# Kernel optimization log

Hardware: AMD Instinct MI355X
Metric: run time of the kernel (lower is better)

Reference implementation:

```python
import jax, jax.numpy as jnp
import numpy as np

D_MODEL = 1024
N_HEADS = 16
D_HEAD = D_MODEL // N_HEADS
SCALE = D_HEAD ** -0.5


def setup_inputs() -> dict:
    key = jax.random.key(0)
    ks = jax.random.split(key, 9)
    s = 0.02
    x = jax.random.normal(ks[0], (2, 2048, D_MODEL), dtype=jnp.float32)
    Wq = jax.random.normal(ks[1], (D_MODEL, D_MODEL), dtype=jnp.float32) * s
    Wk = jax.random.normal(ks[2], (D_MODEL, D_MODEL), dtype=jnp.float32) * s
    Wv = jax.random.normal(ks[3], (D_MODEL, D_MODEL), dtype=jnp.float32) * s
    Wo = jax.random.normal(ks[4], (D_MODEL, D_MODEL), dtype=jnp.float32) * s
    bq = jax.random.normal(ks[5], (D_MODEL,), dtype=jnp.float32) * s
    bk = jax.random.normal(ks[6], (D_MODEL,), dtype=jnp.float32) * s
    bv = jax.random.normal(ks[7], (D_MODEL,), dtype=jnp.float32) * s
    bo = jax.random.normal(ks[8], (D_MODEL,), dtype=jnp.float32) * s
    return {"x": x, "Wq": Wq, "bq": bq, "Wk": Wk, "bk": bk,
            "Wv": Wv, "bv": bv, "Wo": Wo, "bo": bo}


def reference(x, Wq, bq, Wk, bk, Wv, bv, Wo, bo):
    B, S, _ = x.shape
    # torch nn.Linear: y = x @ W.T + b
    def proj(W, b):
        h = jnp.einsum('bsd,ed->bse', x, W) + b
        return h.reshape(B, S, N_HEADS, D_HEAD).transpose(0, 2, 1, 3)  # [B,H,S,Dh]
    Q = proj(Wq, bq)
    K = proj(Wk, bk)
    V = proj(Wv, bv)
    # chunked QK^T softmax over full K == full attention (no mask, dropout=0)
    scores = jnp.einsum('bhqd,bhkd->bhqk', Q, K) * SCALE  # [B,H,S,S]
    attn = jax.nn.softmax(scores, axis=-1)
    out = jnp.einsum('bhqk,bhkd->bhqd', attn, V)
    out = out.transpose(0, 2, 1, 3).reshape(B, S, D_MODEL)
    return jnp.einsum('bsd,ed->bse', out, Wo) + bo
```

## Files before the change

### kernel.cpp

```cpp
#include <hip/hip_runtime.h>
#include <cstdint>
#include <cstddef>


typedef unsigned short u16;
typedef unsigned int u32;
typedef __bf16 bf16x8 __attribute__((ext_vector_type(8)));
typedef float f32x4 __attribute__((ext_vector_type(4)));

#define GLOAD_LDS16(gp, lp)                                                            \
  __builtin_amdgcn_global_load_lds((const __attribute__((address_space(1))) void*)(gp),\
                                   (__attribute__((address_space(3))) void*)(lp),      \
                                   16, 0, 0)

__device__ __forceinline__ u16 f2bf(float f) {
  unsigned u = __builtin_bit_cast(unsigned, f);
  u = u + 0x7fffu + ((u >> 16) & 1u);
  return (u16)(u >> 16);
}

__device__ __forceinline__ u32 pack_bf2(float a, float b) {
  u32 ua = __builtin_bit_cast(u32, a) + 0x8000u;
  u32 ub = __builtin_bit_cast(u32, b) + 0x8000u;
  return __builtin_amdgcn_perm(ub, ua, 0x07060302u);
}

#define QSCALE 0.1803368801111204f

__global__ void cvt_all(const float* __restrict__ x,
                        const float* __restrict__ wq, const float* __restrict__ wk,
                        const float* __restrict__ wv, const float* __restrict__ wo,
                        u16* __restrict__ xb, u16* __restrict__ wqb,
                        u16* __restrict__ wkb, u16* __restrict__ wvb,
                        u16* __restrict__ wob) {
  int bx = blockIdx.x;
  const float* s; u16* d; int off;
  if (bx < 2048)      { s = x;  d = xb;  off = bx; }
  else if (bx < 2560) { s = wq; d = wqb; off = bx - 2048; }
  else if (bx < 3072) { s = wk; d = wkb; off = bx - 2560; }
  else if (bx < 3584) { s = wv; d = wvb; off = bx - 3072; }
  else                { s = wo; d = wob; off = bx - 3584; }
  int i = off * 2048 + threadIdx.x * 8;
  float4 a = *(const float4*)(s + i);
  float4 b = *(const float4*)(s + i + 4);
  uint4 o;
  o.x = f2bf(a.x) | ((u32)f2bf(a.y) << 16);
  o.y = f2bf(a.z) | ((u32)f2bf(a.w) << 16);
  o.z = f2bf(b.x) | ((u32)f2bf(b.y) << 16);
  o.w = f2bf(b.z) | ((u32)f2bf(b.w) << 16);
  *(uint4*)(d + i) = o;
}

template <int MODE>
__global__ __launch_bounds__(256, 3) void gemm_mfma(
    const u16* __restrict__ A,
    const u16* __restrict__ W0, const u16* __restrict__ W1, const u16* __restrict__ W2,
    const float* __restrict__ b0, const float* __restrict__ b1, const float* __restrict__ b2,
    u16* __restrict__ o0, u16* __restrict__ o1, u16* __restrict__ o2,
    float* __restrict__ oF)
{
  __shared__ __align__(16) u16 As[128 * 64];
  __shared__ __align__(16) u16 Bs[128 * 64];

  const int tid = threadIdx.x;
  const int w = tid >> 6, l = tid & 63;
  const int lane = l & 15, quad = l >> 4;
  const int wm = w >> 1, wn = w & 1;
  const int m0 = blockIdx.y * 128;
  const int n0g = blockIdx.x * 128;

  const int src = (MODE == 0) ? (n0g >> 10) : 0;
  const u16* Wsel = (MODE == 0) ? (src == 0 ? W0 : (src == 1 ? W1 : W2)) : W0;
  const float* bsel = (MODE == 0) ? (src == 0 ? b0 : (src == 1 ? b1 : b2)) : b0;
  const int n_base = (MODE == 0) ? (n0g & 1023) : n0g;

  const int c8 = ((l & 7) ^ (l >> 3)) * 8;

  f32x4 acc[4][4] = {};

  for (int kt = 0; kt < 1024; kt += 64) {
    __syncthreads();
    const u16* Ag = A + (size_t)m0 * 1024 + kt;
    const u16* Bg = Wsel + (size_t)n_base * 1024 + kt;
    #pragma unroll
    for (int i = 0; i < 4; ++i) {
      int rr = w * 32 + i * 8;
      GLOAD_LDS16(Ag + (size_t)(rr + (l >> 3)) * 1024 + c8, As + rr * 64);
      GLOAD_LDS16(Bg + (size_t)(rr + (l >> 3)) * 1024 + c8, Bs + rr * 64);
    }
    __syncthreads();

    bf16x8 af[4][2], bf[4][2];
    #pragma unroll
    for (int mf = 0; mf < 4; ++mf)
      #pragma unroll
      for (int ks = 0; ks < 2; ++ks) {
        af[mf][ks] = *(const bf16x8*)((const char*)As +
            (wm * 64 + mf * 16 + lane) * 128 + (((ks * 4 + quad) ^ (lane & 7)) * 16));
        bf[mf][ks] = *(const bf16x8*)((const char*)Bs +
            (wn * 64 + mf * 16 + lane) * 128 + (((ks * 4 + quad) ^ (lane & 7)) * 16));
      }
    #pragma unroll
    for (int ks = 0; ks < 2; ++ks)
      #pragma unroll
      for (int mf = 0; mf < 4; ++mf)
        #pragma unroll
        for (int nf = 0; nf < 4; ++nf)
          acc[mf][nf] = __builtin_amdgcn_mfma_f32_16x16x32_bf16(
              af[mf][ks], bf[nf][ks], acc[mf][nf], 0, 0, 0);
  }

  float bb[4];
  #pragma unroll
  for (int nf = 0; nf < 4; ++nf) bb[nf] = bsel[n_base + wn * 64 + nf * 16 + lane];

  u16* osel = (MODE == 0) ? (src == 0 ? o0 : (src == 1 ? o1 : o2)) : o0;

  #pragma unroll
  for (int mf = 0; mf < 4; ++mf) {
    int mb = m0 + wm * 64 + mf * 16 + quad * 4;
    #pragma unroll
    for (int nf = 0; nf < 4; ++nf) {
      int n_l = wn * 64 + nf * 16 + lane;
      if (MODE == 0 && src == 2) {
        float v0 = acc[mf][nf][0] + bb[nf];
        float v1 = acc[mf][nf][1] + bb[nf];
        float v2 = acc[mf][nf][2] + bb[nf];
        float v3 = acc[mf][nf][3] + bb[nf];
        int bi = mb >> 11, s = mb & 2047;
        int n_in = n_base + n_l;
        int h = n_in >> 6, dh = n_in & 63;
        uint2 pk = make_uint2(pack_bf2(v0, v1), pack_bf2(v2, v3));
        *(uint2*)(o2 + (((size_t)(bi * 16 + h) * 64 + dh) * 2048 + s)) = pk;
      } else {
        #pragma unroll
        for (int r = 0; r < 4; ++r) {
          float v = acc[mf][nf][r] + bb[nf];
          int m = mb + r;
          if (MODE == 0) {
            if (src == 0) v *= QSCALE;
            int bi = m >> 11, s = m & 2047;
            int n_in = n_base + n_l;
            int h = n_in >> 6, dh = n_in & 63;
            osel[(((size_t)(bi * 16 + h) * 2048 + s) << 6) + dh] = f2bf(v);
          } else {
            oF[(size_t)m * 1024 + n0g + n_l] = v;
          }
        }
      }
    }
  }
}

union SMemU {
  struct {
    u16 K[2][64 * 64];
    u16 V[2][64 * 64];
    u16 P[4][32 * 64];
  } m;
  struct {
    float O[4][32 * 64];
    float L[4][32];
  } f;
};

__global__ __launch_bounds__(512, 4) void attn_mfma(
    const u16* __restrict__ Qg_, const u16* __restrict__ Kg_,
    const u16* __restrict__ VTg_, u16* __restrict__ Og)
{
  __shared__ __align__(16) SMemU sm;

  const int tid = threadIdx.x;
  const int w = tid >> 6, l = tid & 63;
  const int lane = l & 15, quad = l >> 4;
  const int g = w >> 1;
  const int kh = w & 1;
  const int bh = blockIdx.y;
  const int q0 = blockIdx.x * 128;

  const u16* Qg  = Qg_ + ((size_t)bh * 2048 + q0 + g * 32) * 64;
  const u16* Kg  = Kg_ + (size_t)bh * 2048 * 64;
  const u16* VTg = VTg_ + (size_t)bh * 64 * 2048;

  const int c8 = ((l & 7) ^ (l >> 3)) * 8;
  const int lrow = l >> 3;
  const int rr = w * 8;

  bf16x8 bq[2][2];
  #pragma unroll
  for (int qf = 0; qf < 2; ++qf)
    #pragma unroll
    for (int ks = 0; ks < 2; ++ks)
      bq[qf][ks] = *(const bf16x8*)(Qg +
          (size_t)(qf * 16 + lane) * 64 + ks * 32 + quad * 8);

  GLOAD_LDS16(Kg + (size_t)(rr + lrow) * 64 + c8, sm.m.K[0] + rr * 64);
  GLOAD_LDS16(VTg + (size_t)(rr + lrow) * 2048 + c8, sm.m.V[0] + rr * 64);

  f32x4 oa[2][4] = {};
  float lsum[2] = {0.f, 0.f};
  u16* Pp = sm.m.P[g];

  for (int kt = 0; kt < 32; ++kt) {
    const int buf = kt & 1;
    __syncthreads();

    if (kt < 31) {
      GLOAD_LDS16(Kg + (size_t)((kt + 1) * 64 + rr + lrow) * 64 + c8,
                  sm.m.K[buf ^ 1] + rr * 64);
      GLOAD_LDS16(VTg + (size_t)(rr + lrow) * 2048 + (kt + 1) * 64 + c8,
                  sm.m.V[buf ^ 1] + rr * 64);
    }

    f32x4 sa[2][2] = {};
    #pragma unroll
    for (int ks = 0; ks < 2; ++ks) {
      bf16x8 ak[2];
      #pragma unroll
      for (int kf = 0; kf < 2; ++kf)
        ak[kf] = *(const bf16x8*)((const char*)sm.m.K[buf] +
            (kh * 32 + kf * 16 + lane) * 128 + (((ks * 4 + quad) ^ (lane & 7)) * 16));
      #pragma unroll
      for (int kf = 0; kf < 2; ++kf)
        #pragma unroll
        for (int qf = 0; qf < 2; ++qf)
          sa[kf][qf] = __builtin_amdgcn_mfma_f32_16x16x32_bf16(
              ak[kf], bq[qf][ks], sa[kf][qf], 0, 0, 0);
    }

    #pragma unroll
    for (int qf = 0; qf < 2; ++qf) {
      int qrow = qf * 16 + lane;
      #pragma unroll
      for (int kf = 0; kf < 2; ++kf) {
        float p0 = __builtin_amdgcn_exp2f(sa[kf][qf][0]);
        float p1 = __builtin_amdgcn_exp2f(sa[kf][qf][1]);
        float p2 = __builtin_amdgcn_exp2f(sa[kf][qf][2]);
        float p3 = __builtin_amdgcn_exp2f(sa[kf][qf][3]);
        lsum[qf] += (p0 + p1) + (p2 + p3);
        int c = kh * 4 + kf * 2 + (quad >> 1);
        *(uint2*)((char*)Pp + qrow * 128 + ((c ^ (lane & 7)) * 16) + (quad & 1) * 8)
            = make_uint2(pack_bf2(p0, p1), pack_bf2(p2, p3));
      }
    }

    {
      bf16x8 bv[4];
      #pragma unroll
      for (int df = 0; df < 4; ++df)
        bv[df] = *(const bf16x8*)((const char*)sm.m.V[buf] +
            (df * 16 + lane) * 128 + (((kh * 4 + quad) ^ (lane & 7)) * 16));
      bf16x8 ap[2];
      #pragma unroll
      for (int qf = 0; qf < 2; ++qf)
        ap[qf] = *(const bf16x8*)((const char*)Pp +
            (qf * 16 + lane) * 128 + (((kh * 4 + quad) ^ (lane & 7)) * 16));
      #pragma unroll
      for (int qf = 0; qf < 2; ++qf)
        #pragma unroll
        for (int df = 0; df < 4; ++df)
          oa[qf][df] = __builtin_amdgcn_mfma_f32_16x16x32_bf16(
              ap[qf], bv[df], oa[qf][df], 0, 0, 0);
    }
  }

  #pragma unroll
  for (int qf = 0; qf < 2; ++qf) {
    lsum[qf] += __shfl_xor(lsum[qf], 16);
    lsum[qf] += __shfl_xor(lsum[qf], 32);
  }

  __syncthreads();
  if (kh == 1) {
    #pragma unroll
    for (int qf = 0; qf < 2; ++qf)
      #pragma unroll
      for (int df = 0; df < 4; ++df)
        #pragma unroll
        for (int r = 0; r < 4; ++r)
          sm.f.O[g][(qf * 16 + quad * 4 + r) * 64 + df * 16 + lane] = oa[qf][df][r];
    if (l < 16) {
      sm.f.L[g][l] = lsum[0];
      sm.f.L[g][16 + l] = lsum[1];
    }
  }
  __syncthreads();
  if (kh == 0) {
    const int b = bh >> 4, hh = bh & 15;
    u16* Ob = Og + ((size_t)b * 2048 + q0 + g * 32) * 1024 + hh * 64;
    float ltot[2];
    #pragma unroll
    for (int qf = 0; qf < 2; ++qf)
      ltot[qf] = lsum[qf] + sm.f.L[g][qf * 16 + lane];
    #pragma unroll
    for (int qf = 0; qf < 2; ++qf)
      #pragma unroll
      for (int r = 0; r < 4; ++r) {
        float inv = 1.0f / __shfl(ltot[qf], quad * 4 + r, 16);
        int qrow = qf * 16 + quad * 4 + r;
        #pragma unroll
        for (int df = 0; df < 4; ++df) {
          float v = oa[qf][df][r] + sm.f.O[g][qrow * 64 + df * 16 + lane];
          Ob[(size_t)qrow * 1024 + df * 16 + lane] = f2bf(v * inv);
        }
      }
  }
}

extern "C" void kernel_launch(void* const* d_in, const int* in_sizes, int n_in,
                              void* d_out, int out_size, void* d_ws, size_t ws_size,
                              hipStream_t stream)
{
  (void)in_sizes; (void)n_in; (void)out_size; (void)ws_size;
  const float* x  = (const float*)d_in[0];
  const float* Wq = (const float*)d_in[1];
  const float* bq = (const float*)d_in[2];
  const float* Wk = (const float*)d_in[3];
  const float* bk = (const float*)d_in[4];
  const float* Wv = (const float*)d_in[5];
  const float* bv = (const float*)d_in[6];
  const float* Wo = (const float*)d_in[7];
  const float* bo = (const float*)d_in[8];
  float* y = (float*)d_out;

  const size_t NM = (size_t)4096 * 1024;
  u16* xb  = (u16*)d_ws;
  u16* wqb = xb + NM;
  u16* wkb = wqb + 1024 * 1024;
  u16* wvb = wkb + 1024 * 1024;
  u16* wob = wvb + 1024 * 1024;
  u16* Qb  = wob + 1024 * 1024;
  u16* Kb  = Qb + NM;
  u16* VTb = Kb + NM;
  u16* AOb = VTb + NM;

  cvt_all<<<4096, 256, 0, stream>>>(x, Wq, Wk, Wv, Wo, xb, wqb, wkb, wvb, wob);

  gemm_mfma<0><<<dim3(24, 32), 256, 0, stream>>>(
      xb, wqb, wkb, wvb, bq, bk, bv, Qb, Kb, VTb, nullptr);

  attn_mfma<<<dim3(16, 32), 512, 0, stream>>>(Qb, Kb, VTb, AOb);

  gemm_mfma<1><<<dim3(8, 32), 256, 0, stream>>>(
      AOb, wob, nullptr, nullptr, bo, nullptr, nullptr,
      nullptr, nullptr, nullptr, y);
}
```

Before: 183.8 us.

## Use 512-thread GEMM blocks with smaller per-wave tiles and 64-row output GEMM

The GEMM kernel now runs 8 waves per block instead of 4, so each wave computes a 32xN sub-tile with fewer accumulators and loads fragments per k-step instead of all at once. This lowers register pressure and raises wave-level parallelism. The output projection switches to 64-row M tiles, doubling its grid so more CUs are used for that small GEMM. In exchange each wave reuses less data per LDS read and the extra waves add synchronization overhead.

```diff
diff --git a/kernel.cpp b/kernel.cpp
--- a/kernel.cpp
+++ b/kernel.cpp
@@ -51,22 +51,26 @@
   *(uint4*)(d + i) = o;
 }
 
-template <int MODE>
-__global__ __launch_bounds__(256, 3) void gemm_mfma(
+template <int MODE, int MT>
+__global__ __launch_bounds__(512, 4) void gemm_mfma(
     const u16* __restrict__ A,
     const u16* __restrict__ W0, const u16* __restrict__ W1, const u16* __restrict__ W2,
     const float* __restrict__ b0, const float* __restrict__ b1, const float* __restrict__ b2,
     u16* __restrict__ o0, u16* __restrict__ o1, u16* __restrict__ o2,
     float* __restrict__ oF)
 {
-  __shared__ __align__(16) u16 As[128 * 64];
+  constexpr int NF = (MT == 128) ? 4 : 2;
+  __shared__ __align__(16) u16 As[MT * 64];
   __shared__ __align__(16) u16 Bs[128 * 64];
 
   const int tid = threadIdx.x;
   const int w = tid >> 6, l = tid & 63;
   const int lane = l & 15, quad = l >> 4;
-  const int wm = w >> 1, wn = w & 1;
-  const int m0 = blockIdx.y * 128;
+  const int wm = (MT == 128) ? (w >> 1) : (w >> 2);
+  const int wn = (MT == 128) ? (w & 1) : (w & 3);
+  const int m_off = wm * 32;
+  const int n_off = wn * (NF * 16);
+  const int m0 = blockIdx.y * MT;
   const int n0g = blockIdx.x * 128;
 
   const int src = (MODE == 0) ? (n0g >> 10) : 0;
@@ -75,53 +79,64 @@
   const int n_base = (MODE == 0) ? (n0g & 1023) : n0g;
 
   const int c8 = ((l & 7) ^ (l >> 3)) * 8;
-
-  f32x4 acc[4][4] = {};
+  const int lrow = l >> 3;
+
+  f32x4 acc[2][NF] = {};
 
   for (int kt = 0; kt < 1024; kt += 64) {
     __syncthreads();
     const u16* Ag = A + (size_t)m0 * 1024 + kt;
     const u16* Bg = Wsel + (size_t)n_base * 1024 + kt;
-    #pragma unroll
-    for (int i = 0; i < 4; ++i) {
-      int rr = w * 32 + i * 8;
-      GLOAD_LDS16(Ag + (size_t)(rr + (l >> 3)) * 1024 + c8, As + rr * 64);
-      GLOAD_LDS16(Bg + (size_t)(rr + (l >> 3)) * 1024 + c8, Bs + rr * 64);
+    if (MT == 128) {
+      #pragma unroll
+      for (int i = 0; i < 2; ++i) {
+        int rr = w * 16 + i * 8;
+        GLOAD_LDS16(Ag + (size_t)(rr + lrow) * 1024 + c8, As + rr * 64);
+      }
+    } else {
+      int rr = w * 8;
+      GLOAD_LDS16(Ag + (size_t)(rr + lrow) * 1024 + c8, As + rr * 64);
+    }
+    #pragma unroll
+    for (int i = 0; i < 2; ++i) {
+      int rr = w * 16 + i * 8;
+      GLOAD_LDS16(Bg + (size_t)(rr + lrow) * 1024 + c8, Bs + rr * 64);
     }
     __syncthreads();
 
-    bf16x8 af[4][2], bf[4][2];
-    #pragma unroll
-    for (int mf = 0; mf < 4; ++mf)
-      #pragma unroll
-      for (int ks = 0; ks < 2; ++ks) {
-        af[mf][ks] = *(const bf16x8*)((const char*)As +
-            (wm * 64 + mf * 16 + lane) * 128 + (((ks * 4 + quad) ^ (lane & 7)) * 16));
-        bf[mf][ks] = *(const bf16x8*)((const char*)Bs +
-            (wn * 64 + mf * 16 + lane) * 128 + (((ks * 4 + quad) ^ (lane & 7)) * 16));
-      }
-    #pragma unroll
-    for (int ks = 0; ks < 2; ++ks)
-      #pragma unroll
-      for (int mf = 0; mf < 4; ++mf)
-        #pragma unroll
-        for (int nf = 0; nf < 4; ++nf)
+    #pragma unroll
+    for (int ks = 0; ks < 2; ++ks) {
+      bf16x8 af[2], bf[NF];
+      #pragma unroll
+      for (int mf = 0; mf < 2; ++mf)
+        af[mf] = *(const bf16x8*)((const char*)As +
+            (m_off + mf * 16 + lane) * 128 + (((ks * 4 + quad) ^ (lane & 7)) * 16));
+      #pragma unroll
+      for (int nf = 0; nf < NF; ++nf)
+        bf[nf] = *(const bf16x8*)((const char*)Bs +
+            (n_off + nf * 16 + lane) * 128 + (((ks * 4 + quad) ^ (lane & 7)) * 16));
+      #pragma unroll
+      for (int mf = 0; mf < 2; ++mf)
+        #pragma unroll
+        for (int nf = 0; nf < NF; ++nf)
           acc[mf][nf] = __builtin_amdgcn_mfma_f32_16x16x32_bf16(
-              af[mf][ks], bf[nf][ks], acc[mf][nf], 0, 0, 0);
-  }
-
-  float bb[4];
+              af[mf], bf[nf], acc[mf][nf], 0, 0, 0);
+    }
+  }
+
+  float bb[NF];
   #pragma unroll
-  for (int nf = 0; nf < 4; ++nf) bb[nf] = bsel[n_base + wn * 64 + nf * 16 + lane];
+  for (int nf = 0; nf < NF; ++nf)
+    bb[nf] = bsel[n_base + n_off + nf * 16 + lane];
 
   u16* osel = (MODE == 0) ? (src == 0 ? o0 : (src == 1 ? o1 : o2)) : o0;
 
   #pragma unroll
-  for (int mf = 0; mf < 4; ++mf) {
-    int mb = m0 + wm * 64 + mf * 16 + quad * 4;
-    #pragma unroll
-    for (int nf = 0; nf < 4; ++nf) {
-      int n_l = wn * 64 + nf * 16 + lane;
+  for (int mf = 0; mf < 2; ++mf) {
+    int mb = m0 + m_off + mf * 16 + quad * 4;
+    #pragma unroll
+    for (int nf = 0; nf < NF; ++nf) {
+      int n_l = n_off + nf * 16 + lane;
       if (MODE == 0 && src == 2) {
         float v0 = acc[mf][nf][0] + bb[nf];
         float v1 = acc[mf][nf][1] + bb[nf];
@@ -336,12 +351,12 @@
 
   cvt_all<<<4096, 256, 0, stream>>>(x, Wq, Wk, Wv, Wo, xb, wqb, wkb, wvb, wob);
 
-  gemm_mfma<0><<<dim3(24, 32), 256, 0, stream>>>(
+  gemm_mfma<0, 128><<<dim3(24, 32), 512, 0, stream>>>(
       xb, wqb, wkb, wvb, bq, bk, bv, Qb, Kb, VTb, nullptr);
 
   attn_mfma<<<dim3(16, 32), 512, 0, stream>>>(Qb, Kb, VTb, AOb);
 
-  gemm_mfma<1><<<dim3(8, 32), 256, 0, stream>>>(
+  gemm_mfma<1, 64><<<dim3(8, 64), 512, 0, stream>>>(
       AOb, wob, nullptr, nullptr, bo, nullptr, nullptr,
       nullptr, nullptr, nullptr, y);
 }
```

New measurement: 188.1 us. +2.3%, slower.
